# Performance work log

Measured on AMD Instinct MI355X. Metric: run time of the kernel, lower is better.

The kernel has to match this reference:

```python
import jax, jax.numpy as jnp
import numpy as np

STATE_DIM, ACTION_DIM, HIDDEN_DIM = 12, 4, 16  # hidden_dim must equal state_dim+action_dim
LN_EPS = 1e-5


def setup_inputs() -> dict:
    key = jax.random.key(0)
    ks = jax.random.split(key, 12)
    B, T = 8192, 256
    D = STATE_DIM + ACTION_DIM  # 16
    H = HIDDEN_DIM
    s = 1.0 / np.sqrt(D)
    sh = 1.0 / np.sqrt(H)
    return {
        "initial_state": jax.random.normal(ks[0], (B, 1, STATE_DIM), jnp.float32),
        "commands": jax.random.normal(ks[1], (B, T, ACTION_DIM), jnp.float32),
        "ln_gamma": jnp.ones((D,), jnp.float32),
        "ln_beta": jnp.zeros((D,), jnp.float32),
        "W_in": jax.random.uniform(ks[2], (H, D), jnp.float32, -s, s),
        "b_in": jax.random.uniform(ks[3], (H,), jnp.float32, -s, s),
        "W_ih": jax.random.uniform(ks[4], (4 * H, D), jnp.float32, -sh, sh),  # LSTM input_size = D
        "W_hh": jax.random.uniform(ks[5], (4 * H, H), jnp.float32, -sh, sh),
        "b_ih": jax.random.uniform(ks[6], (4 * H,), jnp.float32, -sh, sh),
        "b_hh": jax.random.uniform(ks[7], (4 * H,), jnp.float32, -sh, sh),
        "W_out": jax.random.uniform(ks[8], (STATE_DIM, H), jnp.float32, -sh, sh),
        "b_out": jax.random.uniform(ks[9], (STATE_DIM,), jnp.float32, -sh, sh),
    }


def _normalize_sincos(state, cos_idx, sin_idx):
    sn, cs = state[:, sin_idx], state[:, cos_idx]
    norm = jnp.sqrt(sn * sn + cs * cs) + 1e-8
    return state.at[:, sin_idx].set(sn / norm).at[:, cos_idx].set(cs / norm)


def _forward(initial_state, commands, ln_gamma, ln_beta, W_in, b_in,
             W_ih, W_hh, b_ih, b_hh, W_out, b_out):
    B = initial_state.shape[0]
    H = W_hh.shape[1]
    state0 = initial_state[:, 0, :]  # (B, S)
    h0 = jnp.zeros((B, H), initial_state.dtype)
    c0 = jnp.zeros((B, H), initial_state.dtype)

    def step(carry, cmd_t):
        state, h, c = carry
        x = jnp.concatenate([state, cmd_t], axis=-1)          # (B, D)
        mu = jnp.mean(x, axis=-1, keepdims=True)
        var = jnp.mean((x - mu) ** 2, axis=-1, keepdims=True)
        x = (x - mu) * jax.lax.rsqrt(var + LN_EPS) * ln_gamma + ln_beta
        x = x @ W_in.T + b_in                                  # (B, H)
        gates = x @ W_ih.T + b_ih + h @ W_hh.T + b_hh          # (B, 4H)
        i, f, g, o = jnp.split(gates, 4, axis=-1)
        c = jax.nn.sigmoid(f) * c + jax.nn.sigmoid(i) * jnp.tanh(g)
        h = jax.nn.sigmoid(o) * jnp.tanh(c)
        state = state + h @ W_out.T + b_out                    # (B, S)
        state = _normalize_sincos(state, 1, 2)
        state = _normalize_sincos(state, 3, 4)
        state = _normalize_sincos(state, 5, 6)
        return (state, h, c), state

    _, outs = jax.lax.scan(step, (state0, h0, c0), jnp.swapaxes(commands, 0, 1))
    return jnp.swapaxes(outs, 0, 1)  # (B, T, S)


def reference(initial_state, commands, ln_gamma, ln_beta, W_in, b_in,
              W_ih, W_hh, b_ih, b_hh, W_out, b_out):
    return _forward(initial_state, commands, ln_gamma, ln_beta, W_in, b_in,
                    W_ih, W_hh, b_ih, b_hh, W_out, b_out)
```

## Files before the change

### kernel.cpp

```cpp
#include <hip/hip_runtime.h>

typedef float f32x2 __attribute__((ext_vector_type(2)));
typedef float f32x4 __attribute__((ext_vector_type(4)));

#define LOG2E 1.44269504088896340736f

__device__ __forceinline__ float rcp_fast(float x) { return __builtin_amdgcn_rcpf(x); }

__device__ __forceinline__ f32x2 mk2(float a, float b) { f32x2 v; v[0] = a; v[1] = b; return v; }

__device__ __forceinline__ float sigmoid_fast(float x) {
    return rcp_fast(1.0f + __builtin_amdgcn_exp2f(-LOG2E * x));
}

__device__ __forceinline__ float tanh_fast(float x) {
    float a = __builtin_fabsf(x);
    float t = __builtin_amdgcn_exp2f(-2.0f * LOG2E * a);
    float r = (1.0f - t) * rcp_fast(1.0f + t);
    return __builtin_copysignf(r, x);
}

__device__ __forceinline__ void load_pairs16(const float* p, f32x2* dst) {
    const f32x4* q4 = (const f32x4*)p;
    f32x4 a = q4[0], b = q4[1], c = q4[2], d = q4[3];
    dst[0] = __builtin_shufflevector(a, a, 0, 1);
    dst[1] = __builtin_shufflevector(a, a, 2, 3);
    dst[2] = __builtin_shufflevector(b, b, 0, 1);
    dst[3] = __builtin_shufflevector(b, b, 2, 3);
    dst[4] = __builtin_shufflevector(c, c, 0, 1);
    dst[5] = __builtin_shufflevector(c, c, 2, 3);
    dst[6] = __builtin_shufflevector(d, d, 0, 1);
    dst[7] = __builtin_shufflevector(d, d, 2, 3);
}

__global__ __launch_bounds__(64, 2) void vm_kernel(
    const float* __restrict__ init_state,
    const float* __restrict__ commands,
    const float* __restrict__ ln_g,
    const float* __restrict__ ln_b,
    const float* __restrict__ W_in,
    const float* __restrict__ b_in,
    const float* __restrict__ W_ih,
    const float* __restrict__ W_hh,
    const float* __restrict__ b_ih,
    const float* __restrict__ b_hh,
    const float* __restrict__ W_out,
    const float* __restrict__ b_out,
    float* __restrict__ out,
    int B, int T)
{
    const int lane = threadIdx.x;
    const int j = lane & 15;
    const int g = lane >> 4;
    const int b = blockIdx.x * 4 + g;

    __shared__ __align__(16) float sh_x[4][24];
    __shared__ __align__(16) float sh_h[4][24];

    f32x2 Wih[4][8], Wh[4][8];
#pragma unroll
    for (int q = 0; q < 4; ++q) {
        load_pairs16(W_ih + (q * 16 + j) * 16, Wih[q]);
        load_pairs16(W_hh + (q * 16 + j) * 16, Wh[q]);
    }

    f32x2 Wgx[4][8];
    float binacc[4];
#pragma unroll
    for (int q = 0; q < 4; ++q) {
        binacc[q] = 0.0f;
#pragma unroll
        for (int k2 = 0; k2 < 8; ++k2) Wgx[q][k2] = mk2(0.0f, 0.0f);
    }
#pragma unroll
    for (int m = 0; m < 16; ++m) {
        f32x2 wm[8];
        load_pairs16(W_in + m * 16, wm);
        float bm = b_in[m];
#pragma unroll
        for (int q = 0; q < 4; ++q) {
            float wim = Wih[q][m >> 1][m & 1];
            f32x2 w2 = mk2(wim, wim);
#pragma unroll
            for (int k2 = 0; k2 < 8; ++k2) Wgx[q][k2] += w2 * wm[k2];
            binacc[q] += wim * bm;
        }
    }
    float sg[4], cst[4];
    {
        f32x2 gg2[8], bt2[8];
        load_pairs16(ln_g, gg2);
        load_pairs16(ln_b, bt2);
#pragma unroll
        for (int q = 0; q < 4; ++q) {
            f32x2 ss = mk2(0.0f, 0.0f), cc = mk2(0.0f, 0.0f);
#pragma unroll
            for (int k2 = 0; k2 < 8; ++k2) {
                cc += Wgx[q][k2] * bt2[k2];
                Wgx[q][k2] *= gg2[k2];
                ss += Wgx[q][k2];
            }
            sg[q]  = ss[0] + ss[1];
            cst[q] = cc[0] + cc[1] + binacc[q] + b_ih[q * 16 + j] + b_hh[q * 16 + j];
        }
    }

    const bool is_state = (j < 12);
    f32x2 Wo[8];
    float bo = 0.0f;
#pragma unroll
    for (int k2 = 0; k2 < 8; ++k2) Wo[k2] = mk2(0.0f, 0.0f);
    if (is_state) {
        load_pairs16(W_out + j * 16, Wo);
        bo = b_out[j];
    }

    float st = is_state ? init_state[b * 12 + j] : 0.0f;
    float c = 0.0f;
    f32x2 hp[8];
#pragma unroll
    for (int k2 = 0; k2 < 8; ++k2) hp[k2] = mk2(0.0f, 0.0f);

    const float* cmd_ptr = commands + (size_t)b * T * 4 + (j >= 12 ? j - 12 : 0);
    float* out_ptr = out + (size_t)b * T * 12 + j;

    int pj = j;
    if (j >= 1 && j <= 6) pj = ((j - 1) ^ 1) + 1;
    const float* ppart = &sh_x[g][pj];
    const bool donorm = (j >= 1 && j <= 6);

    float cmd0 = (j >= 12) ? cmd_ptr[0] : 0.0f;
    sh_x[g][j] = is_state ? st : cmd0;
    f32x2 xp[8];
    load_pairs16(&sh_x[g][0], xp);

    float mu, inv;
    {
        f32x2 s2 = ((xp[0] + xp[1]) + (xp[2] + xp[3])) + ((xp[4] + xp[5]) + (xp[6] + xp[7]));
        float sum = s2[0] + s2[1];
        f32x2 qq = xp[0] * xp[0];
#pragma unroll
        for (int k2 = 1; k2 < 8; ++k2) qq += xp[k2] * xp[k2];
        float sumsq = qq[0] + qq[1];
        mu = sum * 0.0625f;
        float var = sumsq * 0.0625f - mu * mu;
        inv = __builtin_amdgcn_rsqf(var + 1e-5f);
    }

    float cmdS = (j >= 12) ? cmd_ptr[4] : 0.0f;
    float cmdN = (j >= 12) ? cmd_ptr[8] : 0.0f;

    for (int t = 0; t < T; ++t) {
        f32x2 ai = Wgx[0][0] * xp[0], af = Wgx[1][0] * xp[0];
        f32x2 ag = Wgx[2][0] * xp[0], ao = Wgx[3][0] * xp[0];
        f32x2 hi = Wh[0][0] * hp[0], hf = Wh[1][0] * hp[0];
        f32x2 hg = Wh[2][0] * hp[0], ho = Wh[3][0] * hp[0];
#pragma unroll
        for (int k2 = 1; k2 < 8; ++k2) {
            ai += Wgx[0][k2] * xp[k2]; af += Wgx[1][k2] * xp[k2];
            ag += Wgx[2][k2] * xp[k2]; ao += Wgx[3][k2] * xp[k2];
            hi += Wh[0][k2] * hp[k2];  hf += Wh[1][k2] * hp[k2];
            hg += Wh[2][k2] * hp[k2];  ho += Wh[3][k2] * hp[k2];
        }
        float nmi = -mu * inv;
        float gi = __builtin_fmaf(ai[0] + ai[1], inv, __builtin_fmaf(nmi, sg[0], cst[0] + (hi[0] + hi[1])));
        float gf = __builtin_fmaf(af[0] + af[1], inv, __builtin_fmaf(nmi, sg[1], cst[1] + (hf[0] + hf[1])));
        float gG = __builtin_fmaf(ag[0] + ag[1], inv, __builtin_fmaf(nmi, sg[2], cst[2] + (hg[0] + hg[1])));
        float go = __builtin_fmaf(ao[0] + ao[1], inv, __builtin_fmaf(nmi, sg[3], cst[3] + (ho[0] + ho[1])));

        float iv = sigmoid_fast(gi);
        float fv = sigmoid_fast(gf);
        float gv = tanh_fast(gG);
        float ov = sigmoid_fast(go);
        c = fv * c + iv * gv;
        float hv = ov * tanh_fast(c);

        sh_h[g][j] = hv;
        load_pairs16(&sh_h[g][0], hp);

        f32x2 o2 = Wo[0] * hp[0];
#pragma unroll
        for (int k2 = 1; k2 < 8; ++k2) o2 += Wo[k2] * hp[k2];
        float st_raw = st + (o2[0] + o2[1]) + bo;

        sh_x[g][j] = is_state ? st_raw : cmdS;
        float pv = *ppart;
        load_pairs16(&sh_x[g][0], xp);

        float nrm = __builtin_amdgcn_sqrtf(st_raw * st_raw + pv * pv) + 1e-8f;
        float stn = st_raw * rcp_fast(nrm);
        st = donorm ? stn : st_raw;
        if (is_state) out_ptr[0] = st;
        out_ptr += 12;

        {
            float a = xp[0][1], bq = xp[1][0];
            float r = rcp_fast(__builtin_amdgcn_sqrtf(a * a + bq * bq) + 1e-8f);
            xp[0][1] = a * r; xp[1][0] = bq * r;
        }
        {
            float a = xp[1][1], bq = xp[2][0];
            float r = rcp_fast(__builtin_amdgcn_sqrtf(a * a + bq * bq) + 1e-8f);
            xp[1][1] = a * r; xp[2][0] = bq * r;
        }
        {
            float a = xp[2][1], bq = xp[3][0];
            float r = rcp_fast(__builtin_amdgcn_sqrtf(a * a + bq * bq) + 1e-8f);
            xp[2][1] = a * r; xp[3][0] = bq * r;
        }

        f32x2 s2 = ((xp[0] + xp[1]) + (xp[2] + xp[3])) + ((xp[4] + xp[5]) + (xp[6] + xp[7]));
        float sum = s2[0] + s2[1];
        f32x2 qq = xp[0] * xp[0];
#pragma unroll
        for (int k2 = 1; k2 < 8; ++k2) qq += xp[k2] * xp[k2];
        float sumsq = qq[0] + qq[1];
        mu = sum * 0.0625f;
        float var = sumsq * 0.0625f - mu * mu;
        inv = __builtin_amdgcn_rsqf(var + 1e-5f);

        cmdS = cmdN;
        int tn = t + 3;
        if (tn > T - 1) tn = T - 1;
        if (j >= 12) cmdN = cmd_ptr[(size_t)tn * 4];
    }
}

extern "C" void kernel_launch(void* const* d_in, const int* in_sizes, int n_in,
                              void* d_out, int out_size, void* d_ws, size_t ws_size,
                              hipStream_t stream) {
    const float* init_state = (const float*)d_in[0];
    const float* commands   = (const float*)d_in[1];
    const float* ln_g       = (const float*)d_in[2];
    const float* ln_b       = (const float*)d_in[3];
    const float* W_in       = (const float*)d_in[4];
    const float* b_in       = (const float*)d_in[5];
    const float* W_ih       = (const float*)d_in[6];
    const float* W_hh       = (const float*)d_in[7];
    const float* b_ih       = (const float*)d_in[8];
    const float* b_hh       = (const float*)d_in[9];
    const float* W_out      = (const float*)d_in[10];
    const float* b_out      = (const float*)d_in[11];

    int B = in_sizes[0] / 12;
    int T = in_sizes[1] / (B * 4);

    int blocks = B / 4;
    vm_kernel<<<blocks, 64, 0, stream>>>(init_state, commands, ln_g, ln_b,
                                         W_in, b_in, W_ih, W_hh, b_ih, b_hh,
                                         W_out, b_out, (float*)d_out, B, T);
}
```

Before: 364.1 us.

## Interleave two independent batch streams per wave to hide recurrence latency

Each 64-lane block now processes eight batch rows as two independent streams (P and Q) instead of four. The per-timestep phases of the two streams are interleaved so the dependent latency chains (LDS round trips, transcendentals) of one stream can overlap with the arithmetic of the other. The weight registers are shared between the streams, the grid is halved and launch bounds drop to one wave per EU to make room for the doubled per-stream state. Risks are higher register pressure and fewer resident waves, which could reduce the latency hiding the hardware already provides.

```diff
diff --git a/kernel.cpp b/kernel.cpp
--- a/kernel.cpp
+++ b/kernel.cpp
@@ -33,7 +33,14 @@
     dst[7] = __builtin_shufflevector(d, d, 2, 3);
 }
 
-__global__ __launch_bounds__(64, 2) void vm_kernel(
+struct Stream {
+    float st, c, mu, inv, cmdS, cmdN;
+    f32x2 hp[8], xp[8];
+    const float* cmd_ptr;
+    float* out_ptr;
+};
+
+__global__ __launch_bounds__(64, 1) void vm_kernel(
     const float* __restrict__ init_state,
     const float* __restrict__ commands,
     const float* __restrict__ ln_g,
@@ -52,10 +59,11 @@
     const int lane = threadIdx.x;
     const int j = lane & 15;
     const int g = lane >> 4;
-    const int b = blockIdx.x * 4 + g;
-
-    __shared__ __align__(16) float sh_x[4][24];
-    __shared__ __align__(16) float sh_h[4][24];
+    const int bP = blockIdx.x * 8 + g;
+    const int bQ = bP + 4;
+
+    __shared__ __align__(16) float shxP[4][24], shhP[4][24];
+    __shared__ __align__(16) float shxQ[4][24], shhQ[4][24];
 
     f32x2 Wih[4][8], Wh[4][8];
 #pragma unroll
@@ -115,114 +123,133 @@
         bo = b_out[j];
     }
 
-    float st = is_state ? init_state[b * 12 + j] : 0.0f;
-    float c = 0.0f;
-    f32x2 hp[8];
-#pragma unroll
-    for (int k2 = 0; k2 < 8; ++k2) hp[k2] = mk2(0.0f, 0.0f);
-
-    const float* cmd_ptr = commands + (size_t)b * T * 4 + (j >= 12 ? j - 12 : 0);
-    float* out_ptr = out + (size_t)b * T * 12 + j;
-
     int pj = j;
     if (j >= 1 && j <= 6) pj = ((j - 1) ^ 1) + 1;
-    const float* ppart = &sh_x[g][pj];
     const bool donorm = (j >= 1 && j <= 6);
-
-    float cmd0 = (j >= 12) ? cmd_ptr[0] : 0.0f;
-    sh_x[g][j] = is_state ? st : cmd0;
-    f32x2 xp[8];
-    load_pairs16(&sh_x[g][0], xp);
-
-    float mu, inv;
-    {
-        f32x2 s2 = ((xp[0] + xp[1]) + (xp[2] + xp[3])) + ((xp[4] + xp[5]) + (xp[6] + xp[7]));
+    const float* ppartP = &shxP[g][pj];
+    const float* ppartQ = &shxQ[g][pj];
+
+
+    auto init_stream = [&](Stream& S, int b, float* shx) {
+        S.st = is_state ? init_state[b * 12 + j] : 0.0f;
+        S.c = 0.0f;
+#pragma unroll
+        for (int k2 = 0; k2 < 8; ++k2) S.hp[k2] = mk2(0.0f, 0.0f);
+        S.cmd_ptr = commands + (size_t)b * T * 4 + (j >= 12 ? j - 12 : 0);
+        S.out_ptr = out + (size_t)b * T * 12 + j;
+        float cmd0 = (j >= 12) ? S.cmd_ptr[0] : 0.0f;
+        shx[j] = is_state ? S.st : cmd0;
+        load_pairs16(shx, S.xp);
+        f32x2 s2 = ((S.xp[0] + S.xp[1]) + (S.xp[2] + S.xp[3])) +
+                   ((S.xp[4] + S.xp[5]) + (S.xp[6] + S.xp[7]));
         float sum = s2[0] + s2[1];
-        f32x2 qq = xp[0] * xp[0];
-#pragma unroll
-        for (int k2 = 1; k2 < 8; ++k2) qq += xp[k2] * xp[k2];
+        f32x2 qq = S.xp[0] * S.xp[0];
+#pragma unroll
+        for (int k2 = 1; k2 < 8; ++k2) qq += S.xp[k2] * S.xp[k2];
         float sumsq = qq[0] + qq[1];
-        mu = sum * 0.0625f;
-        float var = sumsq * 0.0625f - mu * mu;
-        inv = __builtin_amdgcn_rsqf(var + 1e-5f);
-    }
-
-    float cmdS = (j >= 12) ? cmd_ptr[4] : 0.0f;
-    float cmdN = (j >= 12) ? cmd_ptr[8] : 0.0f;
-
-    for (int t = 0; t < T; ++t) {
-        f32x2 ai = Wgx[0][0] * xp[0], af = Wgx[1][0] * xp[0];
-        f32x2 ag = Wgx[2][0] * xp[0], ao = Wgx[3][0] * xp[0];
-        f32x2 hi = Wh[0][0] * hp[0], hf = Wh[1][0] * hp[0];
-        f32x2 hg = Wh[2][0] * hp[0], ho = Wh[3][0] * hp[0];
+        S.mu = sum * 0.0625f;
+        float var = sumsq * 0.0625f - S.mu * S.mu;
+        S.inv = __builtin_amdgcn_rsqf(var + 1e-5f);
+        S.cmdS = (j >= 12) ? S.cmd_ptr[4] : 0.0f;
+        S.cmdN = (j >= 12) ? S.cmd_ptr[8] : 0.0f;
+    };
+
+    auto phase_gates = [&](Stream& S) -> float {
+        f32x2 ai = Wgx[0][0] * S.xp[0], af = Wgx[1][0] * S.xp[0];
+        f32x2 ag = Wgx[2][0] * S.xp[0], ao = Wgx[3][0] * S.xp[0];
+        f32x2 hi = Wh[0][0] * S.hp[0], hf = Wh[1][0] * S.hp[0];
+        f32x2 hg = Wh[2][0] * S.hp[0], ho = Wh[3][0] * S.hp[0];
 #pragma unroll
         for (int k2 = 1; k2 < 8; ++k2) {
-            ai += Wgx[0][k2] * xp[k2]; af += Wgx[1][k2] * xp[k2];
-            ag += Wgx[2][k2] * xp[k2]; ao += Wgx[3][k2] * xp[k2];
-            hi += Wh[0][k2] * hp[k2];  hf += Wh[1][k2] * hp[k2];
-            hg += Wh[2][k2] * hp[k2];  ho += Wh[3][k2] * hp[k2];
-        }
-        float nmi = -mu * inv;
-        float gi = __builtin_fmaf(ai[0] + ai[1], inv, __builtin_fmaf(nmi, sg[0], cst[0] + (hi[0] + hi[1])));
-        float gf = __builtin_fmaf(af[0] + af[1], inv, __builtin_fmaf(nmi, sg[1], cst[1] + (hf[0] + hf[1])));
-        float gG = __builtin_fmaf(ag[0] + ag[1], inv, __builtin_fmaf(nmi, sg[2], cst[2] + (hg[0] + hg[1])));
-        float go = __builtin_fmaf(ao[0] + ao[1], inv, __builtin_fmaf(nmi, sg[3], cst[3] + (ho[0] + ho[1])));
-
+            ai += Wgx[0][k2] * S.xp[k2]; af += Wgx[1][k2] * S.xp[k2];
+            ag += Wgx[2][k2] * S.xp[k2]; ao += Wgx[3][k2] * S.xp[k2];
+            hi += Wh[0][k2] * S.hp[k2];  hf += Wh[1][k2] * S.hp[k2];
+            hg += Wh[2][k2] * S.hp[k2];  ho += Wh[3][k2] * S.hp[k2];
+        }
+        float nmi = -S.mu * S.inv;
+        float gi = __builtin_fmaf(ai[0] + ai[1], S.inv, __builtin_fmaf(nmi, sg[0], cst[0] + (hi[0] + hi[1])));
+        float gf = __builtin_fmaf(af[0] + af[1], S.inv, __builtin_fmaf(nmi, sg[1], cst[1] + (hf[0] + hf[1])));
+        float gG = __builtin_fmaf(ag[0] + ag[1], S.inv, __builtin_fmaf(nmi, sg[2], cst[2] + (hg[0] + hg[1])));
+        float go = __builtin_fmaf(ao[0] + ao[1], S.inv, __builtin_fmaf(nmi, sg[3], cst[3] + (ho[0] + ho[1])));
         float iv = sigmoid_fast(gi);
         float fv = sigmoid_fast(gf);
         float gv = tanh_fast(gG);
         float ov = sigmoid_fast(go);
-        c = fv * c + iv * gv;
-        float hv = ov * tanh_fast(c);
-
-        sh_h[g][j] = hv;
-        load_pairs16(&sh_h[g][0], hp);
-
-        f32x2 o2 = Wo[0] * hp[0];
-#pragma unroll
-        for (int k2 = 1; k2 < 8; ++k2) o2 += Wo[k2] * hp[k2];
-        float st_raw = st + (o2[0] + o2[1]) + bo;
-
-        sh_x[g][j] = is_state ? st_raw : cmdS;
-        float pv = *ppart;
-        load_pairs16(&sh_x[g][0], xp);
-
+        S.c = fv * S.c + iv * gv;
+        return ov * tanh_fast(S.c);
+    };
+
+    auto phase_stage_h = [&](Stream& S, float hv, float* shh) {
+        shh[j] = hv;
+        load_pairs16(shh, S.hp);
+    };
+
+    auto phase_wout_stagex = [&](Stream& S, float* shx, const float* ppart,
+                                 float& st_raw, float& pv) {
+        f32x2 o2 = Wo[0] * S.hp[0];
+#pragma unroll
+        for (int k2 = 1; k2 < 8; ++k2) o2 += Wo[k2] * S.hp[k2];
+        st_raw = S.st + (o2[0] + o2[1]) + bo;
+        shx[j] = is_state ? st_raw : S.cmdS;
+        pv = *ppart;
+        load_pairs16(shx, S.xp);
+    };
+
+    auto phase_finish = [&](Stream& S, float st_raw, float pv, int t) {
         float nrm = __builtin_amdgcn_sqrtf(st_raw * st_raw + pv * pv) + 1e-8f;
         float stn = st_raw * rcp_fast(nrm);
-        st = donorm ? stn : st_raw;
-        if (is_state) out_ptr[0] = st;
-        out_ptr += 12;
+        S.st = donorm ? stn : st_raw;
+        if (is_state) S.out_ptr[0] = S.st;
+        S.out_ptr += 12;
 
         {
-            float a = xp[0][1], bq = xp[1][0];
+            float a = S.xp[0][1], bq = S.xp[1][0];
             float r = rcp_fast(__builtin_amdgcn_sqrtf(a * a + bq * bq) + 1e-8f);
-            xp[0][1] = a * r; xp[1][0] = bq * r;
+            S.xp[0][1] = a * r; S.xp[1][0] = bq * r;
         }
         {
-            float a = xp[1][1], bq = xp[2][0];
+            float a = S.xp[1][1], bq = S.xp[2][0];
             float r = rcp_fast(__builtin_amdgcn_sqrtf(a * a + bq * bq) + 1e-8f);
-            xp[1][1] = a * r; xp[2][0] = bq * r;
+            S.xp[1][1] = a * r; S.xp[2][0] = bq * r;
         }
         {
-            float a = xp[2][1], bq = xp[3][0];
+            float a = S.xp[2][1], bq = S.xp[3][0];
             float r = rcp_fast(__builtin_amdgcn_sqrtf(a * a + bq * bq) + 1e-8f);
-            xp[2][1] = a * r; xp[3][0] = bq * r;
-        }
-
-        f32x2 s2 = ((xp[0] + xp[1]) + (xp[2] + xp[3])) + ((xp[4] + xp[5]) + (xp[6] + xp[7]));
+            S.xp[2][1] = a * r; S.xp[3][0] = bq * r;
+        }
+
+        f32x2 s2 = ((S.xp[0] + S.xp[1]) + (S.xp[2] + S.xp[3])) +
+                   ((S.xp[4] + S.xp[5]) + (S.xp[6] + S.xp[7]));
         float sum = s2[0] + s2[1];
-        f32x2 qq = xp[0] * xp[0];
-#pragma unroll
-        for (int k2 = 1; k2 < 8; ++k2) qq += xp[k2] * xp[k2];
+        f32x2 qq = S.xp[0] * S.xp[0];
+#pragma unroll
+        for (int k2 = 1; k2 < 8; ++k2) qq += S.xp[k2] * S.xp[k2];
         float sumsq = qq[0] + qq[1];
-        mu = sum * 0.0625f;
-        float var = sumsq * 0.0625f - mu * mu;
-        inv = __builtin_amdgcn_rsqf(var + 1e-5f);
-
-        cmdS = cmdN;
+        S.mu = sum * 0.0625f;
+        float var = sumsq * 0.0625f - S.mu * S.mu;
+        S.inv = __builtin_amdgcn_rsqf(var + 1e-5f);
+
+        S.cmdS = S.cmdN;
         int tn = t + 3;
         if (tn > T - 1) tn = T - 1;
-        if (j >= 12) cmdN = cmd_ptr[(size_t)tn * 4];
+        if (j >= 12) S.cmdN = S.cmd_ptr[(size_t)tn * 4];
+    };
+
+    Stream P, Q;
+    init_stream(P, bP, &shxP[g][0]);
+    init_stream(Q, bQ, &shxQ[g][0]);
+
+    for (int t = 0; t < T; ++t) {
+        float hvP = phase_gates(P);
+        phase_stage_h(P, hvP, &shhP[g][0]);
+        float hvQ = phase_gates(Q);
+        phase_stage_h(Q, hvQ, &shhQ[g][0]);
+        float strP, pvP;
+        phase_wout_stagex(P, &shxP[g][0], ppartP, strP, pvP);
+        float strQ, pvQ;
+        phase_wout_stagex(Q, &shxQ[g][0], ppartQ, strQ, pvQ);
+        phase_finish(P, strP, pvP, t);
+        phase_finish(Q, strQ, pvQ, t);
     }
 }
 
@@ -245,7 +272,7 @@
     int B = in_sizes[0] / 12;
     int T = in_sizes[1] / (B * 4);
 
-    int blocks = B / 4;
+    int blocks = B / 8;
     vm_kernel<<<blocks, 64, 0, stream>>>(init_state, commands, ln_g, ln_b,
                                          W_in, b_in, W_ih, W_hh, b_ih, b_hh,
                                          W_out, b_out, (float*)d_out, B, T);
```

After: 446.3 us. +22.6%, slower.

## Split each LSTM row's K-dimension across two half-waves with swizzle reduction

Applied to the files above, without the earlier changes.

Each batch element now uses 32 lanes instead of 16: the 16-wide reduction dimension is split into two halves of 8, and partial dot products are combined with a ds_swizzle xor-16 exchange. The aim is to shorten the serial per-step dependency chain, to halve per-thread register use, and to raise launch bounds to 4 waves per SIMD. The grid doubles, and work per step now includes extra cross-lane exchanges plus duplicated activation math in both halves.

```diff
diff --git a/kernel.cpp b/kernel.cpp
--- a/kernel.cpp
+++ b/kernel.cpp
@@ -5,35 +5,40 @@
 
 #define LOG2E 1.44269504088896340736f
 
-__device__ __forceinline__ float rcp_fast(float x) { return __builtin_amdgcn_rcpf(x); }
-
-__device__ __forceinline__ f32x2 mk2(float a, float b) { f32x2 v; v[0] = a; v[1] = b; return v; }
-
-__device__ __forceinline__ float sigmoid_fast(float x) {
+static __device__ __forceinline__ float rcp_fast(float x) { return __builtin_amdgcn_rcpf(x); }
+
+static __device__ __forceinline__ f32x2 mk2(float a, float b) { f32x2 v; v[0] = a; v[1] = b; return v; }
+
+static __device__ __forceinline__ float sigmoid_fast(float x) {
     return rcp_fast(1.0f + __builtin_amdgcn_exp2f(-LOG2E * x));
 }
 
-__device__ __forceinline__ float tanh_fast(float x) {
+static __device__ __forceinline__ float tanh_fast(float x) {
     float a = __builtin_fabsf(x);
     float t = __builtin_amdgcn_exp2f(-2.0f * LOG2E * a);
     float r = (1.0f - t) * rcp_fast(1.0f + t);
     return __builtin_copysignf(r, x);
 }
 
-__device__ __forceinline__ void load_pairs16(const float* p, f32x2* dst) {
+static __device__ __forceinline__ float xor16(float v) {
+    return __int_as_float(__builtin_amdgcn_ds_swizzle(__float_as_int(v), 0x401F));
+}
+
+static __device__ __forceinline__ void load_pairs8(const float* p, f32x2* dst) {
     const f32x4* q4 = (const f32x4*)p;
-    f32x4 a = q4[0], b = q4[1], c = q4[2], d = q4[3];
+    f32x4 a = q4[0], b = q4[1];
     dst[0] = __builtin_shufflevector(a, a, 0, 1);
     dst[1] = __builtin_shufflevector(a, a, 2, 3);
     dst[2] = __builtin_shufflevector(b, b, 0, 1);
     dst[3] = __builtin_shufflevector(b, b, 2, 3);
-    dst[4] = __builtin_shufflevector(c, c, 0, 1);
-    dst[5] = __builtin_shufflevector(c, c, 2, 3);
-    dst[6] = __builtin_shufflevector(d, d, 0, 1);
-    dst[7] = __builtin_shufflevector(d, d, 2, 3);
-}
-
-__global__ __launch_bounds__(64, 2) void vm_kernel(
+}
+
+static __device__ __forceinline__ void load_pairs16(const float* p, f32x2* dst) {
+    load_pairs8(p, dst);
+    load_pairs8(p + 8, dst + 4);
+}
+
+__global__ __launch_bounds__(64, 4) void vm_kernel(
     const float* __restrict__ init_state,
     const float* __restrict__ commands,
     const float* __restrict__ ln_g,
@@ -51,122 +56,139 @@
 {
     const int lane = threadIdx.x;
     const int j = lane & 15;
-    const int g = lane >> 4;
-    const int b = blockIdx.x * 4 + g;
-
-    __shared__ __align__(16) float sh_x[4][24];
-    __shared__ __align__(16) float sh_h[4][24];
-
-    f32x2 Wih[4][8], Wh[4][8];
+    const int half = (lane >> 4) & 1;
+    const int g = lane >> 5;
+    const int b = blockIdx.x * 2 + g;
+    const int kb = half * 8;
+    const bool hf0 = (half == 0);
+    const bool is_state = (j < 12);
+
+    __shared__ __align__(16) float shx[2][24];
+    __shared__ __align__(16) float shh[2][24];
+
+    f32x2 Wih[4][8], Wh[4][4];
 #pragma unroll
     for (int q = 0; q < 4; ++q) {
         load_pairs16(W_ih + (q * 16 + j) * 16, Wih[q]);
-        load_pairs16(W_hh + (q * 16 + j) * 16, Wh[q]);
-    }
-
-    f32x2 Wgx[4][8];
+        load_pairs8(W_hh + (q * 16 + j) * 16 + kb, Wh[q]);
+    }
+
+    f32x2 Wgx[4][4];
     float binacc[4];
 #pragma unroll
     for (int q = 0; q < 4; ++q) {
         binacc[q] = 0.0f;
 #pragma unroll
-        for (int k2 = 0; k2 < 8; ++k2) Wgx[q][k2] = mk2(0.0f, 0.0f);
+        for (int k2 = 0; k2 < 4; ++k2) Wgx[q][k2] = mk2(0.0f, 0.0f);
     }
 #pragma unroll
     for (int m = 0; m < 16; ++m) {
-        f32x2 wm[8];
-        load_pairs16(W_in + m * 16, wm);
+        f32x2 wm[4];
+        load_pairs8(W_in + m * 16 + kb, wm);
         float bm = b_in[m];
 #pragma unroll
         for (int q = 0; q < 4; ++q) {
             float wim = Wih[q][m >> 1][m & 1];
             f32x2 w2 = mk2(wim, wim);
 #pragma unroll
-            for (int k2 = 0; k2 < 8; ++k2) Wgx[q][k2] += w2 * wm[k2];
+            for (int k2 = 0; k2 < 4; ++k2) Wgx[q][k2] += w2 * wm[k2];
             binacc[q] += wim * bm;
         }
     }
     float sg[4], cst[4];
     {
-        f32x2 gg2[8], bt2[8];
-        load_pairs16(ln_g, gg2);
-        load_pairs16(ln_b, bt2);
+        f32x2 gg2[4], bt2[4];
+        load_pairs8(ln_g + kb, gg2);
+        load_pairs8(ln_b + kb, bt2);
 #pragma unroll
         for (int q = 0; q < 4; ++q) {
             f32x2 ss = mk2(0.0f, 0.0f), cc = mk2(0.0f, 0.0f);
 #pragma unroll
-            for (int k2 = 0; k2 < 8; ++k2) {
+            for (int k2 = 0; k2 < 4; ++k2) {
                 cc += Wgx[q][k2] * bt2[k2];
                 Wgx[q][k2] *= gg2[k2];
                 ss += Wgx[q][k2];
             }
-            sg[q]  = ss[0] + ss[1];
-            cst[q] = cc[0] + cc[1] + binacc[q] + b_ih[q * 16 + j] + b_hh[q * 16 + j];
-        }
-    }
-
-    const bool is_state = (j < 12);
-    f32x2 Wo[8];
+            float sp = ss[0] + ss[1];
+            float cp = cc[0] + cc[1];
+            sg[q] = sp + xor16(sp);
+            cst[q] = (cp + xor16(cp)) + binacc[q]
+                   + b_ih[q * 16 + j] + b_hh[q * 16 + j];
+        }
+    }
+
+    f32x2 Wo[4];
     float bo = 0.0f;
 #pragma unroll
-    for (int k2 = 0; k2 < 8; ++k2) Wo[k2] = mk2(0.0f, 0.0f);
+    for (int k2 = 0; k2 < 4; ++k2) Wo[k2] = mk2(0.0f, 0.0f);
     if (is_state) {
-        load_pairs16(W_out + j * 16, Wo);
+        load_pairs8(W_out + j * 16 + kb, Wo);
         bo = b_out[j];
     }
 
     float st = is_state ? init_state[b * 12 + j] : 0.0f;
     float c = 0.0f;
-    f32x2 hp[8];
-#pragma unroll
-    for (int k2 = 0; k2 < 8; ++k2) hp[k2] = mk2(0.0f, 0.0f);
+    f32x2 hp[4];
+#pragma unroll
+    for (int k2 = 0; k2 < 4; ++k2) hp[k2] = mk2(0.0f, 0.0f);
 
     const float* cmd_ptr = commands + (size_t)b * T * 4 + (j >= 12 ? j - 12 : 0);
     float* out_ptr = out + (size_t)b * T * 12 + j;
+    const bool do_cmd = hf0 && (j >= 12);
 
     int pj = j;
     if (j >= 1 && j <= 6) pj = ((j - 1) ^ 1) + 1;
-    const float* ppart = &sh_x[g][pj];
+    const float* ppart = &shx[g][pj];
     const bool donorm = (j >= 1 && j <= 6);
 
-    float cmd0 = (j >= 12) ? cmd_ptr[0] : 0.0f;
-    sh_x[g][j] = is_state ? st : cmd0;
-    f32x2 xp[8];
-    load_pairs16(&sh_x[g][0], xp);
+    float cmd0 = do_cmd ? cmd_ptr[0] : 0.0f;
+    if (hf0) shx[g][j] = is_state ? st : cmd0;
+    f32x2 xp[4];
+    load_pairs8(&shx[g][kb], xp);
 
     float mu, inv;
     {
-        f32x2 s2 = ((xp[0] + xp[1]) + (xp[2] + xp[3])) + ((xp[4] + xp[5]) + (xp[6] + xp[7]));
-        float sum = s2[0] + s2[1];
+        f32x2 s2 = (xp[0] + xp[1]) + (xp[2] + xp[3]);
+        float sp = s2[0] + s2[1];
         f32x2 qq = xp[0] * xp[0];
 #pragma unroll
-        for (int k2 = 1; k2 < 8; ++k2) qq += xp[k2] * xp[k2];
-        float sumsq = qq[0] + qq[1];
+        for (int k2 = 1; k2 < 4; ++k2) qq += xp[k2] * xp[k2];
+        float qp = qq[0] + qq[1];
+        float sum = sp + xor16(sp);
+        float sumsq = qp + xor16(qp);
         mu = sum * 0.0625f;
         float var = sumsq * 0.0625f - mu * mu;
         inv = __builtin_amdgcn_rsqf(var + 1e-5f);
     }
 
-    float cmdS = (j >= 12) ? cmd_ptr[4] : 0.0f;
-    float cmdN = (j >= 12) ? cmd_ptr[8] : 0.0f;
+    float cmdS = do_cmd ? cmd_ptr[(size_t)(T > 1 ? 1 : 0) * 4] : 0.0f;
+    float cmdN = do_cmd ? cmd_ptr[(size_t)(T > 2 ? 2 : 0) * 4] : 0.0f;
 
     for (int t = 0; t < T; ++t) {
-        f32x2 ai = Wgx[0][0] * xp[0], af = Wgx[1][0] * xp[0];
-        f32x2 ag = Wgx[2][0] * xp[0], ao = Wgx[3][0] * xp[0];
-        f32x2 hi = Wh[0][0] * hp[0], hf = Wh[1][0] * hp[0];
-        f32x2 hg = Wh[2][0] * hp[0], ho = Wh[3][0] * hp[0];
-#pragma unroll
-        for (int k2 = 1; k2 < 8; ++k2) {
-            ai += Wgx[0][k2] * xp[k2]; af += Wgx[1][k2] * xp[k2];
-            ag += Wgx[2][k2] * xp[k2]; ao += Wgx[3][k2] * xp[k2];
-            hi += Wh[0][k2] * hp[k2];  hf += Wh[1][k2] * hp[k2];
-            hg += Wh[2][k2] * hp[k2];  ho += Wh[3][k2] * hp[k2];
-        }
+        f32x2 a0 = Wgx[0][0] * xp[0], a1 = Wgx[1][0] * xp[0];
+        f32x2 a2 = Wgx[2][0] * xp[0], a3 = Wgx[3][0] * xp[0];
+        f32x2 h0 = Wh[0][0] * hp[0], h1 = Wh[1][0] * hp[0];
+        f32x2 h2 = Wh[2][0] * hp[0], h3 = Wh[3][0] * hp[0];
+#pragma unroll
+        for (int k2 = 1; k2 < 4; ++k2) {
+            a0 += Wgx[0][k2] * xp[k2]; a1 += Wgx[1][k2] * xp[k2];
+            a2 += Wgx[2][k2] * xp[k2]; a3 += Wgx[3][k2] * xp[k2];
+            h0 += Wh[0][k2] * hp[k2];  h1 += Wh[1][k2] * hp[k2];
+            h2 += Wh[2][k2] * hp[k2];  h3 += Wh[3][k2] * hp[k2];
+        }
+        float p0 = __builtin_fmaf(a0[0] + a0[1], inv, h0[0] + h0[1]);
+        float p1 = __builtin_fmaf(a1[0] + a1[1], inv, h1[0] + h1[1]);
+        float p2 = __builtin_fmaf(a2[0] + a2[1], inv, h2[0] + h2[1]);
+        float p3 = __builtin_fmaf(a3[0] + a3[1], inv, h3[0] + h3[1]);
+        float r0 = p0 + xor16(p0);
+        float r1 = p1 + xor16(p1);
+        float r2 = p2 + xor16(p2);
+        float r3 = p3 + xor16(p3);
         float nmi = -mu * inv;
-        float gi = __builtin_fmaf(ai[0] + ai[1], inv, __builtin_fmaf(nmi, sg[0], cst[0] + (hi[0] + hi[1])));
-        float gf = __builtin_fmaf(af[0] + af[1], inv, __builtin_fmaf(nmi, sg[1], cst[1] + (hf[0] + hf[1])));
-        float gG = __builtin_fmaf(ag[0] + ag[1], inv, __builtin_fmaf(nmi, sg[2], cst[2] + (hg[0] + hg[1])));
-        float go = __builtin_fmaf(ao[0] + ao[1], inv, __builtin_fmaf(nmi, sg[3], cst[3] + (ho[0] + ho[1])));
+        float gi = r0 + __builtin_fmaf(nmi, sg[0], cst[0]);
+        float gf = r1 + __builtin_fmaf(nmi, sg[1], cst[1]);
+        float gG = r2 + __builtin_fmaf(nmi, sg[2], cst[2]);
+        float go = r3 + __builtin_fmaf(nmi, sg[3], cst[3]);
 
         float iv = sigmoid_fast(gi);
         float fv = sigmoid_fast(gf);
@@ -175,54 +197,62 @@
         c = fv * c + iv * gv;
         float hv = ov * tanh_fast(c);
 
-        sh_h[g][j] = hv;
-        load_pairs16(&sh_h[g][0], hp);
+        if (hf0) shh[g][j] = hv;
+        load_pairs8(&shh[g][kb], hp);
 
         f32x2 o2 = Wo[0] * hp[0];
 #pragma unroll
-        for (int k2 = 1; k2 < 8; ++k2) o2 += Wo[k2] * hp[k2];
-        float st_raw = st + (o2[0] + o2[1]) + bo;
-
-        sh_x[g][j] = is_state ? st_raw : cmdS;
+        for (int k2 = 1; k2 < 4; ++k2) o2 += Wo[k2] * hp[k2];
+        float po = o2[0] + o2[1];
+        float o = po + xor16(po);
+        float st_raw = st + o + bo;
+
+        if (hf0) shx[g][j] = is_state ? st_raw : cmdS;
         float pv = *ppart;
-        load_pairs16(&sh_x[g][0], xp);
+        load_pairs8(&shx[g][kb], xp);
 
         float nrm = __builtin_amdgcn_sqrtf(st_raw * st_raw + pv * pv) + 1e-8f;
         float stn = st_raw * rcp_fast(nrm);
         st = donorm ? stn : st_raw;
-        if (is_state) out_ptr[0] = st;
+        if (hf0 && is_state) out_ptr[0] = st;
         out_ptr += 12;
 
+        if (hf0) {
+            {
+                float a = xp[0][1], bq = xp[1][0];
+                float r = rcp_fast(__builtin_amdgcn_sqrtf(a * a + bq * bq) + 1e-8f);
+                xp[0][1] = a * r; xp[1][0] = bq * r;
+            }
+            {
+                float a = xp[1][1], bq = xp[2][0];
+                float r = rcp_fast(__builtin_amdgcn_sqrtf(a * a + bq * bq) + 1e-8f);
+                xp[1][1] = a * r; xp[2][0] = bq * r;
+            }
+            {
+                float a = xp[2][1], bq = xp[3][0];
+                float r = rcp_fast(__builtin_amdgcn_sqrtf(a * a + bq * bq) + 1e-8f);
+                xp[2][1] = a * r; xp[3][0] = bq * r;
+            }
+        }
+
         {
-            float a = xp[0][1], bq = xp[1][0];
-            float r = rcp_fast(__builtin_amdgcn_sqrtf(a * a + bq * bq) + 1e-8f);
-            xp[0][1] = a * r; xp[1][0] = bq * r;
-        }
-        {
-            float a = xp[1][1], bq = xp[2][0];
-            float r = rcp_fast(__builtin_amdgcn_sqrtf(a * a + bq * bq) + 1e-8f);
-            xp[1][1] = a * r; xp[2][0] = bq * r;
-        }
-        {
-            float a = xp[2][1], bq = xp[3][0];
-            float r = rcp_fast(__builtin_amdgcn_sqrtf(a * a + bq * bq) + 1e-8f);
-            xp[2][1] = a * r; xp[3][0] = bq * r;
-        }
-
-        f32x2 s2 = ((xp[0] + xp[1]) + (xp[2] + xp[3])) + ((xp[4] + xp[5]) + (xp[6] + xp[7]));
-        float sum = s2[0] + s2[1];
-        f32x2 qq = xp[0] * xp[0];
-#pragma unroll
-        for (int k2 = 1; k2 < 8; ++k2) qq += xp[k2] * xp[k2];
-        float sumsq = qq[0] + qq[1];
-        mu = sum * 0.0625f;
-        float var = sumsq * 0.0625f - mu * mu;
-        inv = __builtin_amdgcn_rsqf(var + 1e-5f);
+            f32x2 s2 = (xp[0] + xp[1]) + (xp[2] + xp[3]);
+            float sp = s2[0] + s2[1];
+            f32x2 qq = xp[0] * xp[0];
+#pragma unroll
+            for (int k2 = 1; k2 < 4; ++k2) qq += xp[k2] * xp[k2];
+            float qp = qq[0] + qq[1];
+            float sum = sp + xor16(sp);
+            float sumsq = qp + xor16(qp);
+            mu = sum * 0.0625f;
+            float var = sumsq * 0.0625f - mu * mu;
+            inv = __builtin_amdgcn_rsqf(var + 1e-5f);
+        }
 
         cmdS = cmdN;
         int tn = t + 3;
         if (tn > T - 1) tn = T - 1;
-        if (j >= 12) cmdN = cmd_ptr[(size_t)tn * 4];
+        if (do_cmd) cmdN = cmd_ptr[(size_t)tn * 4];
     }
 }
 
@@ -245,7 +275,7 @@
     int B = in_sizes[0] / 12;
     int T = in_sizes[1] / (B * 4);
 
-    int blocks = B / 4;
+    int blocks = B / 2;
     vm_kernel<<<blocks, 64, 0, stream>>>(init_state, commands, ln_g, ln_b,
                                          W_in, b_in, W_ih, W_hh, b_ih, b_hh,
                                          W_out, b_out, (float*)d_out, B, T);
```

Result: slower. 519.0 us (+42.5%).

## Use fp16 packed dot products and ds_bpermute gathers instead of LDS round-trips

Applied to the files above, without the earlier changes.

Converts the weight matrices and per-step input and hidden vectors to packed fp16 and computes the gate, output and layernorm sums with v_dot2 fp32-accumulate instructions, roughly halving the arithmetic instruction count. The shared-memory write-then-read exchange of state and hidden vectors across the 16-lane group becomes ds_bpermute gathers. The sincos normalization of the gathered input is now taken from already-normalized state rather than recomputed. Reduced precision in a 256-step recurrence risks accumulating error beyond tolerance, and the gathers issue 16 bpermutes per vector instead of vector LDS loads.

```diff
diff --git a/kernel.cpp b/kernel.cpp
--- a/kernel.cpp
+++ b/kernel.cpp
@@ -2,25 +2,40 @@
 
 typedef float f32x2 __attribute__((ext_vector_type(2)));
 typedef float f32x4 __attribute__((ext_vector_type(4)));
+typedef _Float16 h16x2 __attribute__((ext_vector_type(2)));
+typedef __fp16 fp16x2_raw __attribute__((ext_vector_type(2)));
 
 #define LOG2E 1.44269504088896340736f
 
-__device__ __forceinline__ float rcp_fast(float x) { return __builtin_amdgcn_rcpf(x); }
-
-__device__ __forceinline__ f32x2 mk2(float a, float b) { f32x2 v; v[0] = a; v[1] = b; return v; }
-
-__device__ __forceinline__ float sigmoid_fast(float x) {
+static __device__ __forceinline__ float rcp_fast(float x) { return __builtin_amdgcn_rcpf(x); }
+
+static __device__ __forceinline__ f32x2 mk2(float a, float b) { f32x2 v; v[0] = a; v[1] = b; return v; }
+
+static __device__ __forceinline__ float sigmoid_fast(float x) {
     return rcp_fast(1.0f + __builtin_amdgcn_exp2f(-LOG2E * x));
 }
 
-__device__ __forceinline__ float tanh_fast(float x) {
+static __device__ __forceinline__ float tanh_fast(float x) {
     float a = __builtin_fabsf(x);
     float t = __builtin_amdgcn_exp2f(-2.0f * LOG2E * a);
     float r = (1.0f - t) * rcp_fast(1.0f + t);
     return __builtin_copysignf(r, x);
 }
 
-__device__ __forceinline__ void load_pairs16(const float* p, f32x2* dst) {
+static __device__ __forceinline__ float fdot2(h16x2 a, h16x2 b, float c) {
+#if __has_builtin(__builtin_amdgcn_fdot2)
+    return __builtin_amdgcn_fdot2(a, b, c, false);
+#else
+    return c + (float)(a[0]) * (float)(b[0]) + (float)(a[1]) * (float)(b[1]);
+#endif
+}
+
+static __device__ __forceinline__ h16x2 pk(float a, float b) {
+    fp16x2_raw r = __builtin_amdgcn_cvt_pkrtz(a, b);
+    return __builtin_bit_cast(h16x2, r);
+}
+
+static __device__ __forceinline__ void load_pairs16(const float* p, f32x2* dst) {
     const f32x4* q4 = (const f32x4*)p;
     f32x4 a = q4[0], b = q4[1], c = q4[2], d = q4[3];
     dst[0] = __builtin_shufflevector(a, a, 0, 1);
@@ -53,15 +68,14 @@
     const int j = lane & 15;
     const int g = lane >> 4;
     const int b = blockIdx.x * 4 + g;
-
-    __shared__ __align__(16) float sh_x[4][24];
-    __shared__ __align__(16) float sh_h[4][24];
-
-    f32x2 Wih[4][8], Wh[4][8];
+    const int gbase = (lane & 48) << 2;
+    const bool is_state = (j < 12);
+
+    f32x2 Wih[4][8], Wh32[4][8];
 #pragma unroll
     for (int q = 0; q < 4; ++q) {
         load_pairs16(W_ih + (q * 16 + j) * 16, Wih[q]);
-        load_pairs16(W_hh + (q * 16 + j) * 16, Wh[q]);
+        load_pairs16(W_hh + (q * 16 + j) * 16, Wh32[q]);
     }
 
     f32x2 Wgx[4][8];
@@ -105,68 +119,98 @@
         }
     }
 
-    const bool is_state = (j < 12);
-    f32x2 Wo[8];
+    h16x2 WgxH[4][8], WhH[4][8];
+#pragma unroll
+    for (int q = 0; q < 4; ++q)
+#pragma unroll
+        for (int k2 = 0; k2 < 8; ++k2) {
+            WgxH[q][k2] = pk(Wgx[q][k2][0], Wgx[q][k2][1]);
+            WhH[q][k2]  = pk(Wh32[q][k2][0], Wh32[q][k2][1]);
+        }
+
+    h16x2 WoH[8];
     float bo = 0.0f;
 #pragma unroll
-    for (int k2 = 0; k2 < 8; ++k2) Wo[k2] = mk2(0.0f, 0.0f);
+    for (int k2 = 0; k2 < 8; ++k2) WoH[k2] = pk(0.0f, 0.0f);
     if (is_state) {
-        load_pairs16(W_out + j * 16, Wo);
+        f32x2 wo32[8];
+        load_pairs16(W_out + j * 16, wo32);
+#pragma unroll
+        for (int k2 = 0; k2 < 8; ++k2) WoH[k2] = pk(wo32[k2][0], wo32[k2][1]);
         bo = b_out[j];
     }
+
+    const h16x2 one2 = pk(1.0f, 1.0f);
 
     float st = is_state ? init_state[b * 12 + j] : 0.0f;
     float c = 0.0f;
-    f32x2 hp[8];
-#pragma unroll
-    for (int k2 = 0; k2 < 8; ++k2) hp[k2] = mk2(0.0f, 0.0f);
+    h16x2 hpk[8];
+#pragma unroll
+    for (int k2 = 0; k2 < 8; ++k2) hpk[k2] = pk(0.0f, 0.0f);
 
     const float* cmd_ptr = commands + (size_t)b * T * 4 + (j >= 12 ? j - 12 : 0);
     float* out_ptr = out + (size_t)b * T * 12 + j;
+    const bool do_cmd = (j >= 12);
 
     int pj = j;
     if (j >= 1 && j <= 6) pj = ((j - 1) ^ 1) + 1;
-    const float* ppart = &sh_x[g][pj];
+    const int paddr = ((lane & 48) | pj) << 2;
     const bool donorm = (j >= 1 && j <= 6);
 
-    float cmd0 = (j >= 12) ? cmd_ptr[0] : 0.0f;
-    sh_x[g][j] = is_state ? st : cmd0;
-    f32x2 xp[8];
-    load_pairs16(&sh_x[g][0], xp);
-
+#define GATHER16(v, dst)                                                      \
+    do {                                                                      \
+        int _s = __float_as_int(v);                                           \
+        _Pragma("unroll")                                                     \
+        for (int _i = 0; _i < 16; ++_i)                                       \
+            dst[_i] = __int_as_float(                                         \
+                __builtin_amdgcn_ds_bpermute(gbase + (_i << 2), _s));         \
+    } while (0)
+
+    float cmd0 = do_cmd ? cmd_ptr[0] : 0.0f;
+    h16x2 xpk[8];
     float mu, inv;
     {
-        f32x2 s2 = ((xp[0] + xp[1]) + (xp[2] + xp[3])) + ((xp[4] + xp[5]) + (xp[6] + xp[7]));
-        float sum = s2[0] + s2[1];
-        f32x2 qq = xp[0] * xp[0];
-#pragma unroll
-        for (int k2 = 1; k2 < 8; ++k2) qq += xp[k2] * xp[k2];
-        float sumsq = qq[0] + qq[1];
-        mu = sum * 0.0625f;
-        float var = sumsq * 0.0625f - mu * mu;
+        float xv = is_state ? st : cmd0;
+        float xg[16];
+        GATHER16(xv, xg);
+#pragma unroll
+        for (int i = 0; i < 8; ++i) xpk[i] = pk(xg[2 * i], xg[2 * i + 1]);
+        float s0 = 0.0f, s1 = 0.0f, q0 = 0.0f, q1 = 0.0f;
+#pragma unroll
+        for (int i = 0; i < 4; ++i) {
+            s0 = fdot2(xpk[i], one2, s0);
+            s1 = fdot2(xpk[i + 4], one2, s1);
+            q0 = fdot2(xpk[i], xpk[i], q0);
+            q1 = fdot2(xpk[i + 4], xpk[i + 4], q1);
+        }
+        mu = (s0 + s1) * 0.0625f;
+        float var = (q0 + q1) * 0.0625f - mu * mu;
         inv = __builtin_amdgcn_rsqf(var + 1e-5f);
     }
 
-    float cmdS = (j >= 12) ? cmd_ptr[4] : 0.0f;
-    float cmdN = (j >= 12) ? cmd_ptr[8] : 0.0f;
+    float cmdS = do_cmd ? cmd_ptr[(size_t)(T > 1 ? 1 : 0) * 4] : 0.0f;
+    float cmdN = do_cmd ? cmd_ptr[(size_t)(T > 2 ? 2 : 0) * 4] : 0.0f;
 
     for (int t = 0; t < T; ++t) {
-        f32x2 ai = Wgx[0][0] * xp[0], af = Wgx[1][0] * xp[0];
-        f32x2 ag = Wgx[2][0] * xp[0], ao = Wgx[3][0] * xp[0];
-        f32x2 hi = Wh[0][0] * hp[0], hf = Wh[1][0] * hp[0];
-        f32x2 hg = Wh[2][0] * hp[0], ho = Wh[3][0] * hp[0];
-#pragma unroll
-        for (int k2 = 1; k2 < 8; ++k2) {
-            ai += Wgx[0][k2] * xp[k2]; af += Wgx[1][k2] * xp[k2];
-            ag += Wgx[2][k2] * xp[k2]; ao += Wgx[3][k2] * xp[k2];
-            hi += Wh[0][k2] * hp[k2];  hf += Wh[1][k2] * hp[k2];
-            hg += Wh[2][k2] * hp[k2];  ho += Wh[3][k2] * hp[k2];
+        float gx[4], gh[4];
+#pragma unroll
+        for (int q = 0; q < 4; ++q) {
+            float a0 = 0.0f, a1 = 0.0f, h0 = 0.0f, h1 = 0.0f;
+#pragma unroll
+            for (int k = 0; k < 4; ++k) {
+                a0 = fdot2(WgxH[q][k], xpk[k], a0);
+                a1 = fdot2(WgxH[q][k + 4], xpk[k + 4], a1);
+                h0 = fdot2(WhH[q][k], hpk[k], h0);
+                h1 = fdot2(WhH[q][k + 4], hpk[k + 4], h1);
+            }
+            gx[q] = a0 + a1;
+            gh[q] = h0 + h1;
         }
         float nmi = -mu * inv;
-        float gi = __builtin_fmaf(ai[0] + ai[1], inv, __builtin_fmaf(nmi, sg[0], cst[0] + (hi[0] + hi[1])));
-        float gf = __builtin_fmaf(af[0] + af[1], inv, __builtin_fmaf(nmi, sg[1], cst[1] + (hf[0] + hf[1])));
-        float gG = __builtin_fmaf(ag[0] + ag[1], inv, __builtin_fmaf(nmi, sg[2], cst[2] + (hg[0] + hg[1])));
-        float go = __builtin_fmaf(ao[0] + ao[1], inv, __builtin_fmaf(nmi, sg[3], cst[3] + (ho[0] + ho[1])));
+        float gi = __builtin_fmaf(gx[0], inv, __builtin_fmaf(nmi, sg[0], cst[0] + gh[0]));
+        float gf = __builtin_fmaf(gx[1], inv, __builtin_fmaf(nmi, sg[1], cst[1] + gh[1]));
+        float gG = __builtin_fmaf(gx[2], inv, __builtin_fmaf(nmi, sg[2], cst[2] + gh[2]));
+        float go = __builtin_fmaf(gx[3], inv, __builtin_fmaf(nmi, sg[3], cst[3] + gh[3]));
 
         float iv = sigmoid_fast(gi);
         float fv = sigmoid_fast(gf);
@@ -175,18 +219,23 @@
         c = fv * c + iv * gv;
         float hv = ov * tanh_fast(c);
 
-        sh_h[g][j] = hv;
-        load_pairs16(&sh_h[g][0], hp);
-
-        f32x2 o2 = Wo[0] * hp[0];
-#pragma unroll
-        for (int k2 = 1; k2 < 8; ++k2) o2 += Wo[k2] * hp[k2];
-        float st_raw = st + (o2[0] + o2[1]) + bo;
-
-        sh_x[g][j] = is_state ? st_raw : cmdS;
-        float pv = *ppart;
-        load_pairs16(&sh_x[g][0], xp);
-
+        {
+            float hg[16];
+            GATHER16(hv, hg);
+#pragma unroll
+            for (int i = 0; i < 8; ++i) hpk[i] = pk(hg[2 * i], hg[2 * i + 1]);
+        }
+
+        float o0 = 0.0f, o1 = 0.0f;
+#pragma unroll
+        for (int k = 0; k < 4; ++k) {
+            o0 = fdot2(WoH[k], hpk[k], o0);
+            o1 = fdot2(WoH[k + 4], hpk[k + 4], o1);
+        }
+        float st_raw = st + (o0 + o1) + bo;
+
+        float pv = __int_as_float(
+            __builtin_amdgcn_ds_bpermute(paddr, __float_as_int(st_raw)));
         float nrm = __builtin_amdgcn_sqrtf(st_raw * st_raw + pv * pv) + 1e-8f;
         float stn = st_raw * rcp_fast(nrm);
         st = donorm ? stn : st_raw;
@@ -194,36 +243,30 @@
         out_ptr += 12;
 
         {
-            float a = xp[0][1], bq = xp[1][0];
-            float r = rcp_fast(__builtin_amdgcn_sqrtf(a * a + bq * bq) + 1e-8f);
-            xp[0][1] = a * r; xp[1][0] = bq * r;
-        }
-        {
-            float a = xp[1][1], bq = xp[2][0];
-            float r = rcp_fast(__builtin_amdgcn_sqrtf(a * a + bq * bq) + 1e-8f);
-            xp[1][1] = a * r; xp[2][0] = bq * r;
-        }
-        {
-            float a = xp[2][1], bq = xp[3][0];
-            float r = rcp_fast(__builtin_amdgcn_sqrtf(a * a + bq * bq) + 1e-8f);
-            xp[2][1] = a * r; xp[3][0] = bq * r;
-        }
-
-        f32x2 s2 = ((xp[0] + xp[1]) + (xp[2] + xp[3])) + ((xp[4] + xp[5]) + (xp[6] + xp[7]));
-        float sum = s2[0] + s2[1];
-        f32x2 qq = xp[0] * xp[0];
-#pragma unroll
-        for (int k2 = 1; k2 < 8; ++k2) qq += xp[k2] * xp[k2];
-        float sumsq = qq[0] + qq[1];
-        mu = sum * 0.0625f;
-        float var = sumsq * 0.0625f - mu * mu;
+            float xv = is_state ? st : cmdS;
+            float xg[16];
+            GATHER16(xv, xg);
+#pragma unroll
+            for (int i = 0; i < 8; ++i) xpk[i] = pk(xg[2 * i], xg[2 * i + 1]);
+        }
+        float s0 = 0.0f, s1 = 0.0f, q0 = 0.0f, q1 = 0.0f;
+#pragma unroll
+        for (int i = 0; i < 4; ++i) {
+            s0 = fdot2(xpk[i], one2, s0);
+            s1 = fdot2(xpk[i + 4], one2, s1);
+            q0 = fdot2(xpk[i], xpk[i], q0);
+            q1 = fdot2(xpk[i + 4], xpk[i + 4], q1);
+        }
+        mu = (s0 + s1) * 0.0625f;
+        float var = (q0 + q1) * 0.0625f - mu * mu;
         inv = __builtin_amdgcn_rsqf(var + 1e-5f);
 
         cmdS = cmdN;
         int tn = t + 3;
         if (tn > T - 1) tn = T - 1;
-        if (j >= 12) cmdN = cmd_ptr[(size_t)tn * 4];
-    }
+        if (do_cmd) cmdN = cmd_ptr[(size_t)tn * 4];
+    }
+#undef GATHER16
 }
 
 extern "C" void kernel_launch(void* const* d_in, const int* in_sizes, int n_in,
```

Result: slower. 393.1 us (+8.0%).
